# Performance work log

Hardware: AMD Instinct MI355X
Metric: run time of the kernel (lower is better)

## Reference

```python
import jax, jax.numpy as jnp
import numpy as np

DX = 1.0      # grid spacing
RHO = 1.0     # density
NU = 0.1      # viscosity
DT = 0.1      # timestep
STEPS = 1000  # Jacobi relaxation iterations

# Periodic (CIRCULAR) finite-difference stencils via jnp.roll on the last two axes.

def ddx(f):
    # central difference along x (axis -2)
    return (jnp.roll(f, -1, axis=-2) - jnp.roll(f, 1, axis=-2)) / (2.0 * DX)

def ddy(f):
    # central difference along y (axis -1)
    return (jnp.roll(f, -1, axis=-1) - jnp.roll(f, 1, axis=-1)) / (2.0 * DX)

def neighbor_sum(f):
    # 4-neighbor sum: LapInv stencil used by the Jacobi step
    return (jnp.roll(f, 1, axis=-2) + jnp.roll(f, -1, axis=-2)
            + jnp.roll(f, 1, axis=-1) + jnp.roll(f, -1, axis=-1))

def laplacian(f):
    # 5-point Laplacian / dx^2
    return (neighbor_sum(f) - 4.0 * f) / (DX * DX)


def setup_inputs() -> dict:
    key = jax.random.key(0)
    k1, k2 = jax.random.split(key)
    X = jax.random.normal(k1, (2, 1, 512, 512), dtype=jnp.float32)
    forcing = jax.random.normal(k2, (2, 1, 512, 512), dtype=jnp.float32)
    t = jnp.zeros((), dtype=jnp.float32)
    return {"t": t, "X": X, "forcing": forcing}


def reference(t, X, forcing):
    # advection (v . grad) v : X[0]*dXi/dx + X[1]*dXi/dy, broadcast over vector dim
    adv = X[0] * ddx(X) + X[1] * ddy(X)              # (2, C, H, W)
    partial = -adv + NU * laplacian(X) + forcing      # (2, C, H, W)
    # divergence of partial -> pressure Poisson RHS
    B = RHO * (ddx(partial[0]) + ddy(partial[1])) / DT  # (C, H, W)

    def poisson_jacobi_step(phi, _):
        phi = (neighbor_sum(phi) - B * (DX * DX)) / 4.0
        return phi, None

    phi, _ = jax.lax.scan(poisson_jacobi_step, B, xs=None, length=STEPS)
    grad_phi = jnp.stack([ddx(phi), ddy(phi)])        # (2, C, H, W)
    return partial - grad_phi / RHO
```

## Files before the change

kernel.cpp:

```cpp
#include <hip/hip_runtime.h>
#include <math.h>


#define HH 512
#define WW 512
#define NCELL (HH * WW)
#define NU_C 0.1f
#define PI_F 3.14159265358979323846f
#define PADDED 576

__device__ __forceinline__ int padi(int i) { return i + (i >> 3); }

__device__ __forceinline__ float2 cadd(float2 a, float2 b) { return make_float2(a.x + b.x, a.y + b.y); }
__device__ __forceinline__ float2 csub(float2 a, float2 b) { return make_float2(a.x - b.x, a.y - b.y); }
__device__ __forceinline__ float2 cmul(float2 a, float2 b) {
    return make_float2(a.x * b.x - a.y * b.y, a.x * b.y + a.y * b.x);
}

template <int S>
__device__ __forceinline__ float2 cmul_tw(float2 a, float2 w) {
    float wy = (S < 0) ? w.y : -w.y;
    return make_float2(a.x * w.x - a.y * wy, a.x * wy + a.y * w.x);
}

template <int S>
__device__ __forceinline__ void bfly8(float2 r[8]) {
    const float c = 0.70710678118654752f;
    const float s = (float)S;
    float2 e0 = cadd(r[0], r[4]), f0 = csub(r[0], r[4]);
    float2 e1 = cadd(r[2], r[6]), f1 = csub(r[2], r[6]);
    float2 g0 = cadd(r[1], r[5]), h0 = csub(r[1], r[5]);
    float2 g1 = cadd(r[3], r[7]), h1 = csub(r[3], r[7]);
    float2 E0 = cadd(e0, e1), E2 = csub(e0, e1);
    float2 if1 = make_float2(-s * f1.y, s * f1.x);
    float2 E1 = cadd(f0, if1), E3 = csub(f0, if1);
    float2 O0 = cadd(g0, g1), O2 = csub(g0, g1);
    float2 ih1 = make_float2(-s * h1.y, s * h1.x);
    float2 O1 = cadd(h0, ih1), O3 = csub(h0, ih1);
    float2 t1 = make_float2(c * (O1.x - s * O1.y), c * (O1.y + s * O1.x));
    float2 t2 = make_float2(-s * O2.y, s * O2.x);
    float2 t3 = make_float2(-c * (O3.x + s * O3.y), -c * (O3.y - s * O3.x));
    r[0] = cadd(E0, O0); r[4] = csub(E0, O0);
    r[1] = cadd(E1, t1); r[5] = csub(E1, t1);
    r[2] = cadd(E2, t2); r[6] = csub(E2, t2);
    r[3] = cadd(E3, t3); r[7] = csub(E3, t3);
}

struct Twid { float2 s1[8]; float2 s2[8]; };

__device__ __forceinline__ void make_tw(Twid& tw, int t) {
    float sn, cs;
    sincosf(-2.0f * PI_F * (float)(t & 7) * (1.0f / 64.0f), &sn, &cs);
    float2 T1 = make_float2(cs, sn);
    tw.s1[0] = make_float2(1.0f, 0.0f);
#pragma unroll
    for (int m = 1; m < 8; ++m) tw.s1[m] = cmul(tw.s1[m - 1], T1);
    sincosf(-2.0f * PI_F * (float)t * (1.0f / 512.0f), &sn, &cs);
    float2 T2 = make_float2(cs, sn);
    tw.s2[0] = make_float2(1.0f, 0.0f);
#pragma unroll
    for (int m = 1; m < 8; ++m) tw.s2[m] = cmul(tw.s2[m - 1], T2);
}

template <int S>
__device__ __forceinline__ void fft512(float2 r[8], const Twid& tw,
                                       float2* b0, float2* b1, int t) {
    bfly8<S>(r);
#pragma unroll
    for (int k = 0; k < 8; ++k) b0[padi(8 * t + k)] = r[k];
    __syncthreads();
#pragma unroll
    for (int m = 0; m < 8; ++m) r[m] = b0[padi(t + 64 * m)];
#pragma unroll
    for (int m = 1; m < 8; ++m) r[m] = cmul_tw<S>(r[m], tw.s1[m]);
    bfly8<S>(r);
    int base = ((t >> 3) << 6) + (t & 7);
#pragma unroll
    for (int k = 0; k < 8; ++k) b1[padi(base + 8 * k)] = r[k];
    __syncthreads();
#pragma unroll
    for (int m = 0; m < 8; ++m) r[m] = b1[padi(t + 64 * m)];
#pragma unroll
    for (int m = 1; m < 8; ++m) r[m] = cmul_tw<S>(r[m], tw.s2[m]);
    bfly8<S>(r);
}

__global__ __launch_bounds__(128) void kA(const float* __restrict__ X,
                                          const float* __restrict__ F,
                                          float* __restrict__ p,
                                          float2* __restrict__ Zt) {
    __shared__ float2 b0[2][PADDED], b1[2][PADDED];
    int b = blockIdx.x;
    int w = threadIdx.x >> 6, t = threadIdx.x & 63;
    int i = 2 * b + w;
    Twid tw; make_tw(tw, t);
    int ip = (i + 1) & 511, im = (i + 511) & 511;
    const float* X0 = X;
    const float* X1 = X + NCELL;
    float2 r[8];
#pragma unroll
    for (int m = 0; m < 8; ++m) {
        int j = t + 64 * m;
        int jp = (j + 1) & 511, jm = (j + 511) & 511;
        float x0c = X0[i * WW + j], x1c = X1[i * WW + j];
        float aip = X0[ip * WW + j], aim = X0[im * WW + j];
        float ajp = X0[i * WW + jp], ajm = X0[i * WW + jm];
        float p0 = -(x0c * (aip - aim) * 0.5f + x1c * (ajp - ajm) * 0.5f)
                 + NU_C * (aip + aim + ajp + ajm - 4.0f * x0c) + F[i * WW + j];
        float bip = X1[ip * WW + j], bim = X1[im * WW + j];
        float bjp = X1[i * WW + jp], bjm = X1[i * WW + jm];
        float p1 = -(x0c * (bip - bim) * 0.5f + x1c * (bjp - bjm) * 0.5f)
                 + NU_C * (bip + bim + bjp + bjm - 4.0f * x1c) + F[NCELL + i * WW + j];
        p[i * WW + j] = p0;
        p[NCELL + i * WW + j] = p1;
        r[m] = make_float2(p0, p1);
    }
    fft512<-1>(r, tw, b0[w], b1[w], t);
#pragma unroll
    for (int k = 0; k < 8; ++k) b0[w][t + 64 * k] = r[k];
    __syncthreads();
#pragma unroll
    for (int q = 0; q < 4; ++q) {
        int f = threadIdx.x + 128 * q;
        float2 v0 = b0[0][f], v1 = b0[1][f];
        *reinterpret_cast<float4*>(&Zt[f * 512 + 2 * b]) = make_float4(v0.x, v0.y, v1.x, v1.y);
    }
}

__global__ __launch_bounds__(64) void kB1(const float2* __restrict__ Zt,
                                          float2* __restrict__ S) {
    __shared__ float2 b0[PADDED], b1[PADDED];
    int j = blockIdx.x, t = threadIdx.x;
    Twid tw; make_tw(tw, t);
    float2 r[8];
#pragma unroll
    for (int m = 0; m < 8; ++m) r[m] = Zt[j * 512 + t + 64 * m];
    fft512<-1>(r, tw, b0, b1, t);
#pragma unroll
    for (int k = 0; k < 8; ++k) S[j * 512 + t + 64 * k] = r[k];
}

__global__ __launch_bounds__(128) void kB2(const float2* __restrict__ S,
                                           float2* __restrict__ W1) {
    __shared__ float2 b0[2][PADDED], b1[2][PADDED];
    int b = blockIdx.x;
    int w = threadIdx.x >> 6, t = threadIdx.x & 63;
    int j = 2 * b + w;
    int mj = (512 - j) & 511;
    Twid tw; make_tw(tw, t);

    float shy, chy;
    sincosf(PI_F * (float)j * (1.0f / 512.0f), &shy, &chy);
    float sy = 2.0f * shy * chy;
    float qy = shy * shy;

    float sh, ch;
    sincosf(PI_F * (float)t * (1.0f / 512.0f), &sh, &ch);
    const float c8 = 0.92387953251128675613f;
    const float s8 = 0.38268343236508977173f;

    float2 r[8];
#pragma unroll
    for (int k = 0; k < 8; ++k) {
        int ki = t + 64 * k;
        int mi = (HH - ki) & 511;
        float2 z  = S[j * 512 + ki];
        float2 zc = S[mj * 512 + mi];
        float sx = 2.0f * sh * ch;
        float qx = sh * sh;
        float qs = qx + qy;
        float beta = 0.0f;
        if (ki != 0 || j != 0) {
            float rN;
            if (qs < 1.0f)      rN = expf(1000.0f * log1pf(-qs));
            else if (qs > 1.0f) rN = expf(1000.0f * logf(qs - 1.0f));
            else                rN = 0.0f;
            float M = rN - (1.0f - rN) / (4.0f * qs);
            beta = -10.0f * M * (1.0f / (512.0f * 512.0f));
        }
        float su  = sx * sx + sy * sy;
        float u2x = sx * sx - sy * sy;
        float u2y = 2.0f * sx * sy;
        float cx = zc.x, cy = -zc.y;
        float tx = u2x * cx - u2y * cy;
        float ty = u2x * cy + u2y * cx;
        float bh = 0.5f * beta;
        r[k] = make_float2(bh * (su * z.x + tx), bh * (su * z.y + ty));
        float nch = ch * c8 - sh * s8;
        sh = sh * c8 + ch * s8;
        ch = nch;
    }

    fft512<1>(r, tw, b0[w], b1[w], t);
#pragma unroll
    for (int k = 0; k < 8; ++k) b0[w][t + 64 * k] = r[k];
    __syncthreads();
#pragma unroll
    for (int q = 0; q < 4; ++q) {
        int f = threadIdx.x + 128 * q;
        float2 v0 = b0[0][f], v1 = b0[1][f];
        *reinterpret_cast<float4*>(&W1[f * 512 + 2 * b]) = make_float4(v0.x, v0.y, v1.x, v1.y);
    }
}

__global__ __launch_bounds__(64) void kC(const float2* __restrict__ W1,
                                         const float* __restrict__ p,
                                         float* __restrict__ out) {
    __shared__ float2 b0[PADDED], b1[PADDED];
    int i = blockIdx.x, t = threadIdx.x;
    Twid tw; make_tw(tw, t);
    float2 r[8];
#pragma unroll
    for (int m = 0; m < 8; ++m) r[m] = W1[i * 512 + t + 64 * m];
    fft512<1>(r, tw, b0, b1, t);
#pragma unroll
    for (int k = 0; k < 8; ++k) {
        int j = t + 64 * k;
        float2 w = r[k];
        out[i * WW + j]         = p[i * WW + j]         - w.x;
        out[NCELL + i * WW + j] = p[NCELL + i * WW + j] - w.y;
    }
}

extern "C" void kernel_launch(void* const* d_in, const int* in_sizes, int n_in,
                              void* d_out, int out_size, void* d_ws, size_t ws_size,
                              hipStream_t stream) {
    const float* X = (const float*)d_in[1];
    const float* F = (const float*)d_in[2];
    float* out = (float*)d_out;
    float* ws  = (float*)d_ws;

    float*  p  = ws;
    float2* Zt = (float2*)(ws + 2 * NCELL);
    float2* S  = Zt + NCELL;
    float2* W1 = S + NCELL;

    kA <<<dim3(256), dim3(128), 0, stream>>>(X, F, p, Zt);
    kB1<<<dim3(512), dim3(64),  0, stream>>>(Zt, S);
    kB2<<<dim3(256), dim3(128), 0, stream>>>(S, W1);
    kC <<<dim3(512), dim3(64),  0, stream>>>(W1, p, out);
}
```

Baseline: 77.94 us.

## Fuse four FFT stages into one cooperative kernel with grid syncs

```diff
diff --git a/kernel.cpp b/kernel.cpp
--- a/kernel.cpp
+++ b/kernel.cpp
@@ -1,5 +1,8 @@
 #include <hip/hip_runtime.h>
+#include <hip/hip_cooperative_groups.h>
 #include <math.h>
+
+namespace cg = cooperative_groups;
 
 
 #define HH 512
@@ -8,6 +11,8 @@
 #define NU_C 0.1f
 #define PI_F 3.14159265358979323846f
 #define PADDED 576
+
+typedef float4 f4_a8 __attribute__((aligned(8)));
 
 __device__ __forceinline__ int padi(int i) { return i + (i >> 3); }
 
@@ -85,18 +90,23 @@
     bfly8<S>(r);
 }
 
-__global__ __launch_bounds__(128) void kA(const float* __restrict__ X,
-                                          const float* __restrict__ F,
-                                          float* __restrict__ p,
-                                          float2* __restrict__ Zt) {
-    __shared__ float2 b0[2][PADDED], b1[2][PADDED];
-    int b = blockIdx.x;
-    int w = threadIdx.x >> 6, t = threadIdx.x & 63;
-    int i = 2 * b + w;
+__global__ __launch_bounds__(256) void fused(const float* __restrict__ X,
+                                             const float* __restrict__ F,
+                                             float2* __restrict__ Zt,
+                                             float2* __restrict__ W1,
+                                             float* __restrict__ out) {
+    __shared__ float2 b0[4][PADDED], b1[4][PADDED];
+    cg::grid_group grid = cg::this_grid();
+    const int b = blockIdx.x;
+    const int w = threadIdx.x >> 6;
+    const int t = threadIdx.x & 63;
     Twid tw; make_tw(tw, t);
-    int ip = (i + 1) & 511, im = (i + 511) & 511;
+
+    const int i = 4 * b + w;
+    const int ip = (i + 1) & 511, im = (i + 511) & 511;
     const float* X0 = X;
     const float* X1 = X + NCELL;
+    float p0r[8], p1r[8];
     float2 r[8];
 #pragma unroll
     for (int m = 0; m < 8; ++m) {
@@ -111,8 +121,7 @@
         float bjp = X1[i * WW + jp], bjm = X1[i * WW + jm];
         float p1 = -(x0c * (bip - bim) * 0.5f + x1c * (bjp - bjm) * 0.5f)
                  + NU_C * (bip + bim + bjp + bjm - 4.0f * x1c) + F[NCELL + i * WW + j];
-        p[i * WW + j] = p0;
-        p[NCELL + i * WW + j] = p1;
+        p0r[m] = p0; p1r[m] = p1;
         r[m] = make_float2(p0, p1);
     }
     fft512<-1>(r, tw, b0[w], b1[w], t);
@@ -120,57 +129,48 @@
     for (int k = 0; k < 8; ++k) b0[w][t + 64 * k] = r[k];
     __syncthreads();
 #pragma unroll
-    for (int q = 0; q < 4; ++q) {
-        int f = threadIdx.x + 128 * q;
-        float2 v0 = b0[0][f], v1 = b0[1][f];
-        *reinterpret_cast<float4*>(&Zt[f * 512 + 2 * b]) = make_float4(v0.x, v0.y, v1.x, v1.y);
-    }
-}
-
-__global__ __launch_bounds__(64) void kB1(const float2* __restrict__ Zt,
-                                          float2* __restrict__ S) {
-    __shared__ float2 b0[PADDED], b1[PADDED];
-    int j = blockIdx.x, t = threadIdx.x;
-    Twid tw; make_tw(tw, t);
-    float2 r[8];
-#pragma unroll
-    for (int m = 0; m < 8; ++m) r[m] = Zt[j * 512 + t + 64 * m];
-    fft512<-1>(r, tw, b0, b1, t);
-#pragma unroll
-    for (int k = 0; k < 8; ++k) S[j * 512 + t + 64 * k] = r[k];
-}
-
-__global__ __launch_bounds__(128) void kB2(const float2* __restrict__ S,
-                                           float2* __restrict__ W1) {
-    __shared__ float2 b0[2][PADDED], b1[2][PADDED];
-    int b = blockIdx.x;
-    int w = threadIdx.x >> 6, t = threadIdx.x & 63;
-    int j = 2 * b + w;
-    int mj = (512 - j) & 511;
-    Twid tw; make_tw(tw, t);
+    for (int q = 0; q < 2; ++q) {
+        int f = threadIdx.x + 256 * q;
+        float2 v0 = b0[0][f], v1 = b0[1][f], v2 = b0[2][f], v3 = b0[3][f];
+        *reinterpret_cast<float4*>(&Zt[f * 512 + 4 * b])     = make_float4(v0.x, v0.y, v1.x, v1.y);
+        *reinterpret_cast<float4*>(&Zt[f * 512 + 4 * b + 2]) = make_float4(v2.x, v2.y, v3.x, v3.y);
+    }
+    grid.sync();
+
+    int cw, mw;
+    if (b == 0) {
+        cw = (w == 0) ? 0 : (w == 1) ? 1 : (w == 2) ? 256 : 511;
+        mw = (w == 1) ? 3 : (w == 3) ? 1 : w;
+    } else {
+        cw = (w == 0) ? 2 * b : (w == 1) ? 2 * b + 1 : (w == 2) ? 511 - 2 * b : 512 - 2 * b;
+        mw = w ^ 3;
+    }
+#pragma unroll
+    for (int m = 0; m < 8; ++m) r[m] = Zt[cw * 512 + t + 64 * m];
+    fft512<-1>(r, tw, b0[w], b1[w], t);
+#pragma unroll
+    for (int k = 0; k < 8; ++k) b0[w][t + 64 * k] = r[k];
+    __syncthreads();
 
     float shy, chy;
-    sincosf(PI_F * (float)j * (1.0f / 512.0f), &shy, &chy);
+    sincosf(PI_F * (float)cw * (1.0f / 512.0f), &shy, &chy);
     float sy = 2.0f * shy * chy;
     float qy = shy * shy;
-
     float sh, ch;
     sincosf(PI_F * (float)t * (1.0f / 512.0f), &sh, &ch);
     const float c8 = 0.92387953251128675613f;
     const float s8 = 0.38268343236508977173f;
-
-    float2 r[8];
 #pragma unroll
     for (int k = 0; k < 8; ++k) {
         int ki = t + 64 * k;
         int mi = (HH - ki) & 511;
-        float2 z  = S[j * 512 + ki];
-        float2 zc = S[mj * 512 + mi];
+        float2 z  = r[k];
+        float2 zc = b0[mw][mi];
         float sx = 2.0f * sh * ch;
         float qx = sh * sh;
         float qs = qx + qy;
         float beta = 0.0f;
-        if (ki != 0 || j != 0) {
+        if (ki != 0 || cw != 0) {
             float rN;
             if (qs < 1.0f)      rN = expf(1000.0f * log1pf(-qs));
             else if (qs > 1.0f) rN = expf(1000.0f * logf(qs - 1.0f));
@@ -190,35 +190,37 @@
         sh = sh * c8 + ch * s8;
         ch = nch;
     }
-
+    __syncthreads();
     fft512<1>(r, tw, b0[w], b1[w], t);
 #pragma unroll
     for (int k = 0; k < 8; ++k) b0[w][t + 64 * k] = r[k];
     __syncthreads();
-#pragma unroll
-    for (int q = 0; q < 4; ++q) {
-        int f = threadIdx.x + 128 * q;
-        float2 v0 = b0[0][f], v1 = b0[1][f];
-        *reinterpret_cast<float4*>(&W1[f * 512 + 2 * b]) = make_float4(v0.x, v0.y, v1.x, v1.y);
-    }
-}
-
-__global__ __launch_bounds__(64) void kC(const float2* __restrict__ W1,
-                                         const float* __restrict__ p,
-                                         float* __restrict__ out) {
-    __shared__ float2 b0[PADDED], b1[PADDED];
-    int i = blockIdx.x, t = threadIdx.x;
-    Twid tw; make_tw(tw, t);
-    float2 r[8];
+    {
+        const int cA = 2 * b;
+        const int cB = 511 - 2 * b;
+#pragma unroll
+        for (int q = 0; q < 2; ++q) {
+            int f = threadIdx.x + 256 * q;
+            float2 v0 = b0[0][f], v1 = b0[1][f], v2 = b0[2][f], v3 = b0[3][f];
+            *reinterpret_cast<float4*>(&W1[f * 512 + cA]) = make_float4(v0.x, v0.y, v1.x, v1.y);
+            if (b) {
+                *reinterpret_cast<f4_a8*>(&W1[f * 512 + cB]) = make_float4(v2.x, v2.y, v3.x, v3.y);
+            } else {
+                W1[f * 512 + 256] = v2;
+                W1[f * 512 + 511] = v3;
+            }
+        }
+    }
+    grid.sync();
+
 #pragma unroll
     for (int m = 0; m < 8; ++m) r[m] = W1[i * 512 + t + 64 * m];
-    fft512<1>(r, tw, b0, b1, t);
+    fft512<1>(r, tw, b0[w], b1[w], t);
 #pragma unroll
     for (int k = 0; k < 8; ++k) {
         int j = t + 64 * k;
-        float2 w = r[k];
-        out[i * WW + j]         = p[i * WW + j]         - w.x;
-        out[NCELL + i * WW + j] = p[NCELL + i * WW + j] - w.y;
+        out[i * WW + j]         = p0r[k] - r[k].x;
+        out[NCELL + i * WW + j] = p1r[k] - r[k].y;
     }
 }
 
@@ -230,13 +232,10 @@
     float* out = (float*)d_out;
     float* ws  = (float*)d_ws;
 
-    float*  p  = ws;
-    float2* Zt = (float2*)(ws + 2 * NCELL);
-    float2* S  = Zt + NCELL;
-    float2* W1 = S + NCELL;
-
-    kA <<<dim3(256), dim3(128), 0, stream>>>(X, F, p, Zt);
-    kB1<<<dim3(512), dim3(64),  0, stream>>>(Zt, S);
-    kB2<<<dim3(256), dim3(128), 0, stream>>>(S, W1);
-    kC <<<dim3(512), dim3(64),  0, stream>>>(W1, p, out);
-}
+    float2* Zt = (float2*)ws;
+    float2* W1 = Zt + NCELL;
+
+    void* args[] = {(void*)&X, (void*)&F, (void*)&Zt, (void*)&W1, (void*)&out};
+    hipLaunchCooperativeKernel((const void*)fused, dim3(128), dim3(256),
+                               args, 0, stream);
+}
```

New measurement: 121.6 us. +56.0%, slower.
